# Kernel optimization log

Measured on AMD Instinct MI355X. Metric: run time of the kernel, lower is better.

The kernel has to match this reference:

```python
import jax, jax.numpy as jnp
import numpy as np

B, S, D, L = 16, 512, 256, 8192
DROP_P = 0.2


def setup_inputs() -> dict:
    key = jax.random.key(0)
    k1, k2, k3 = jax.random.split(key, 3)
    x = jax.random.normal(k1, (B, S, D), dtype=jnp.float32)
    label_emb = jax.random.normal(k2, (B, L, D), dtype=jnp.float32)
    mask = jax.random.uniform(k3, (B, S)) < 0.9
    return {"x": x, "mask": mask, "label_emb": label_emb}


def reference(x, mask, label_emb):
    # scores = x @ label_emb^T : [B, S, L]
    scores = jnp.einsum("bsd,bld->bsl", x, label_emb)
    # softmax over label dim (last)
    probs = jax.nn.softmax(scores, axis=-1)
    # post-softmax token masking (non-standard order, faithful to original)
    probs = jnp.where(mask[:, :, None], probs, jnp.zeros((), probs.dtype))
    # dropout (training=True in original), deterministic key for reproducibility
    keep = jax.random.bernoulli(jax.random.key(42), 1.0 - DROP_P, probs.shape)
    probs = jnp.where(keep, probs / (1.0 - DROP_P), jnp.zeros((), probs.dtype))
    # attention pooling: scores^T @ x : [B, L, D]
    return jnp.einsum("bsl,bsd->bld", probs, x)
```

## Files before the change

### kernel.cpp

```cpp
#include <hip/hip_runtime.h>
#include <stdint.h>
#include <stddef.h>

#define B_ 16
#define S_ 512
#define D_ 256
#define L_ 8192

typedef unsigned short u16;
typedef _Float16 f16;
typedef f16 f16x4 __attribute__((ext_vector_type(4)));
typedef f16 f16x8 __attribute__((ext_vector_type(8)));
typedef float f32x4 __attribute__((ext_vector_type(4)));

__device__ __forceinline__ void gl16(const void* g, void* l) {
  __builtin_amdgcn_global_load_lds(
      (const __attribute__((address_space(1))) unsigned int*)g,
      (__attribute__((address_space(3))) unsigned int*)l, 16, 0, 0);
}

__device__ __forceinline__ uint32_t rotl32(uint32_t x, int r) {
  return (x << r) | (x >> (32 - r));
}
__device__ __forceinline__ bool drop_keep(uint32_t j) {
  const uint32_t k0 = 0u, k1 = 42u, k2 = 0x1BD11BDAu ^ k0 ^ k1;
  uint32_t v0 = 0u + k0;
  uint32_t v1 = j + k1;
#define TF_R(r) { v0 += v1; v1 = rotl32(v1, (r)); v1 ^= v0; }
  TF_R(13) TF_R(15) TF_R(26) TF_R(6)
  v0 += k1; v1 += k2 + 1u;
  TF_R(17) TF_R(29) TF_R(16) TF_R(24)
  v0 += k2; v1 += k0 + 2u;
  TF_R(13) TF_R(15) TF_R(26) TF_R(6)
  v0 += k0; v1 += k1 + 3u;
  TF_R(17) TF_R(29) TF_R(16) TF_R(24)
  v0 += k1; v1 += k2 + 4u;
  TF_R(13) TF_R(15) TF_R(26) TF_R(6)
  v0 += k2; v1 += k0 + 5u;
#undef TF_R
  uint32_t bits = v0 ^ v1;
  float u = __uint_as_float((bits >> 9) | 0x3f800000u) - 1.0f;
  return u < 0.8f;
}

__global__ __launch_bounds__(256)
void conv16_kernel(const float* __restrict__ src, f16* __restrict__ dst, int n) {
  int i = (blockIdx.x * 256 + threadIdx.x) * 8;
  if (i >= n) return;
  float4 a = *(const float4*)&src[i];
  float4 b = *(const float4*)&src[i + 4];
  f16x8 o;
  o[0] = (f16)a.x; o[1] = (f16)a.y; o[2] = (f16)a.z; o[3] = (f16)a.w;
  o[4] = (f16)b.x; o[5] = (f16)b.y; o[6] = (f16)b.z; o[7] = (f16)b.w;
  *(f16x8*)&dst[i] = o;
}

__global__ __launch_bounds__(256)
void xt16_kernel(const float* __restrict__ x, f16* __restrict__ xT) {
  const int b = blockIdx.z, sb = blockIdx.x * 32, db = blockIdx.y * 32;
  __shared__ float t[32][33];
  const int tid = threadIdx.x;
  const int r = tid >> 3, c4 = (tid & 7) * 4;
  float4 v = *(const float4*)&x[((size_t)b * S_ + sb + r) * D_ + db + c4];
  t[r][c4] = v.x; t[r][c4 + 1] = v.y; t[r][c4 + 2] = v.z; t[r][c4 + 3] = v.w;
  __syncthreads();
  const int dr = tid >> 3, s4 = (tid & 7) * 4;
  f16x4 o;
#pragma unroll
  for (int j = 0; j < 4; ++j) o[j] = (f16)t[s4 + j][dr];
  *(f16x4*)&xT[((size_t)b * D_ + db + dr) * S_ + sb + s4] = o;
}

__global__ __launch_bounds__(256)
void gemm1t_f16(const f16* __restrict__ eh, const f16* __restrict__ xh,
                float* __restrict__ scoresT, float2* __restrict__ partials,
                uint32_t* __restrict__ kb) {
  __shared__ __align__(16) f16 As[2][4096];
  __shared__ __align__(16) f16 Bs[2][4096];
  __shared__ float pmaxA[128][2];
  __shared__ float psumA[128][2];

  const int tid = threadIdx.x;
  const int lane = tid & 63, wave = tid >> 6;
  const int b = blockIdx.z, lt = blockIdx.x * 128, st = blockIdx.y * 128;

  const int lm = lane & 15, kq = lane >> 4;
  const int wm = (wave & 1) * 64, wn = (wave >> 1) * 64;
  const int ca = (wave & 1) * 4, cb = (wave >> 1) * 4;

  const int srow = lane & 15, sko = (lane >> 4) * 8;
  auto stage = [&](int bi, int k0) {
#pragma unroll
    for (int i = 0; i < 2; ++i) {
      const int c = wave * 2 + i;
      gl16(eh + ((size_t)b * L_ + lt + c * 16 + srow) * D_ + k0 + sko,
           (char*)As[bi] + c * 1024 + lane * 16);
      gl16(xh + ((size_t)b * S_ + st + c * 16 + srow) * D_ + k0 + sko,
           (char*)Bs[bi] + c * 1024 + lane * 16);
    }
  };

  const int q0 = (tid & 1) * 2;
  const int ml = lt + (tid >> 1);
  uint32_t wlo = 0, whi = 0;

  f32x4 acc[4][4] = {};

  stage(0, 0);
  __syncthreads();
  int bi = 0;
  for (int t = 0; t < 8; ++t) {
    if (t < 7) stage(bi ^ 1, (t + 1) * 32);

    {
      const int c = t & 3, q = q0 + (t >> 2);
      const uint32_t base =
          (uint32_t)(b * S_ + st + 32 * c + 8 * q) * (uint32_t)L_ +
          (uint32_t)ml;
      uint32_t byte = 0;
#pragma unroll
      for (int j = 0; j < 8; ++j)
        byte |= (uint32_t)drop_keep(base + (uint32_t)j * L_) << j;
      if (t < 4) wlo |= byte << (8 * c);
      else       whi |= byte << (8 * c);
    }

    f16x8 fa[4], fb[4];
#pragma unroll
    for (int mi = 0; mi < 4; ++mi)
      fa[mi] = *(const f16x8*)&As[bi][((ca + mi) * 64 + kq * 16 + lm) * 8];
#pragma unroll
    for (int ni = 0; ni < 4; ++ni)
      fb[ni] = *(const f16x8*)&Bs[bi][((cb + ni) * 64 + kq * 16 + lm) * 8];
#pragma unroll
    for (int mi = 0; mi < 4; ++mi)
#pragma unroll
      for (int ni = 0; ni < 4; ++ni)
        acc[mi][ni] = __builtin_amdgcn_mfma_f32_16x16x32_f16(
            fa[mi], fb[ni], acc[mi][ni], 0, 0, 0);
    __syncthreads();
    bi ^= 1;
  }

  {
    uint32_t* kp = kb + ((size_t)b * L_ + ml) * 16 + blockIdx.y;
    kp[q0 * 4] = wlo;
    kp[(q0 + 1) * 4] = whi;
  }

#pragma unroll
  for (int mi = 0; mi < 4; ++mi)
#pragma unroll
    for (int ni = 0; ni < 4; ++ni) {
      const int l0 = wm + mi * 16 + kq * 4;
      const int s = wn + ni * 16 + lm;
      float* sp = scoresT + ((size_t)b * L_ + lt + l0) * S_ + st + s;
#pragma unroll
      for (int r = 0; r < 4; ++r) sp[(size_t)r * S_] = acc[mi][ni][r];
    }

  float cmax[4];
#pragma unroll
  for (int ni = 0; ni < 4; ++ni) {
    float v = acc[0][ni][0];
#pragma unroll
    for (int mi = 0; mi < 4; ++mi)
#pragma unroll
      for (int r = 0; r < 4; ++r) v = fmaxf(v, acc[mi][ni][r]);
    cmax[ni] = v;
  }
#pragma unroll
  for (int ni = 0; ni < 4; ++ni) {
    cmax[ni] = fmaxf(cmax[ni], __shfl_xor(cmax[ni], 16, 64));
    cmax[ni] = fmaxf(cmax[ni], __shfl_xor(cmax[ni], 32, 64));
  }
  if (kq == 0) {
#pragma unroll
    for (int ni = 0; ni < 4; ++ni) pmaxA[wn + ni * 16 + lm][wave & 1] = cmax[ni];
  }
  __syncthreads();
  float colm[4];
#pragma unroll
  for (int ni = 0; ni < 4; ++ni) {
    const int s = wn + ni * 16 + lm;
    colm[ni] = fmaxf(pmaxA[s][0], pmaxA[s][1]);
  }
  float psum[4] = {};
#pragma unroll
  for (int ni = 0; ni < 4; ++ni)
#pragma unroll
    for (int mi = 0; mi < 4; ++mi)
#pragma unroll
      for (int r = 0; r < 4; ++r)
        psum[ni] += __expf(acc[mi][ni][r] - colm[ni]);
#pragma unroll
  for (int ni = 0; ni < 4; ++ni) {
    psum[ni] += __shfl_xor(psum[ni], 16, 64);
    psum[ni] += __shfl_xor(psum[ni], 32, 64);
  }
  if (kq == 0) {
#pragma unroll
    for (int ni = 0; ni < 4; ++ni) psumA[wn + ni * 16 + lm][wave & 1] = psum[ni];
  }
  __syncthreads();
  if (tid < 128) {
    float m = fmaxf(pmaxA[tid][0], pmaxA[tid][1]);
    float Z = psumA[tid][0] + psumA[tid][1];
    partials[((size_t)b * 64 + blockIdx.x) * S_ + st + tid] = make_float2(m, Z);
  }
}

__global__ __launch_bounds__(256)
void combine_kernel(const float2* __restrict__ partials,
                    const int* __restrict__ mask, float2* __restrict__ stats) {
  const int idx = blockIdx.x * 256 + threadIdx.x;
  const int b = idx / S_, si = idx - b * S_;
  float m = -3.402823466e38f, Z = 0.f;
  for (int t = 0; t < 64; ++t) {
    float2 p = partials[((size_t)b * 64 + t) * S_ + si];
    if (p.x > m) {
      Z = Z * __expf(m - p.x) + p.y;
      m = p.x;
    } else {
      Z += p.y * __expf(p.x - m);
    }
  }
  float f = (mask[idx] != 0) ? (1.25f / Z) : 0.0f;
  stats[idx] = make_float2(m, f);
}

__global__ __launch_bounds__(512)
void gemm2_fused(const float* __restrict__ scoresT, const f16* __restrict__ xT,
                 const float2* __restrict__ stats,
                 const uint32_t* __restrict__ kb, float* __restrict__ out) {
  __shared__ __align__(16) f16 Bs[2][8192];
  __shared__ float2 stat_s[S_];

  const int tid = threadIdx.x;
  const int lane = tid & 63, wave = tid >> 6;
  const int b = blockIdx.z, lt = blockIdx.x * 128;

  stat_s[tid] = stats[b * S_ + tid];

  const int lm = lane & 15, kq = lane >> 4;
  const int l_loc = wave * 16 + lm;

  const int srow = lane & 15, sko = (lane >> 4) * 8;
  const size_t xb_base = (size_t)b * D_ * S_;
  auto stage = [&](int bi, int k0) {
#pragma unroll
    for (int i = 0; i < 2; ++i) {
      const int c = wave * 2 + i;
      gl16(xT + xb_base + (size_t)(c * 16 + srow) * S_ + k0 + sko,
           (char*)Bs[bi] + c * 1024 + lane * 16);
    }
  };

  const float* srowp =
      scoresT + ((size_t)b * L_ + lt + l_loc) * S_ + kq * 8;

  const uint4 kwv = *(const uint4*)(kb + ((size_t)b * L_ + lt + l_loc) * 16 +
                                    kq * 4);
  const uint32_t kwa[4] = {kwv.x, kwv.y, kwv.z, kwv.w};

  f32x4 acc[16] = {};

  f32x4 sv0 = *(const f32x4*)&srowp[0];
  f32x4 sv1 = *(const f32x4*)&srowp[4];
  stage(0, 0);
  __syncthreads();
#pragma unroll
  for (int kg = 0; kg < 4; ++kg) {
#pragma unroll
    for (int c = 0; c < 4; ++c) {
      const int kk = kg * 4 + c;
      const int k0 = kk * 32;
      const int bi = kk & 1;
      f32x4 nv0, nv1;
      if (kk < 15) {
        stage(bi ^ 1, k0 + 32);
        nv0 = *(const f32x4*)&srowp[k0 + 32];
        nv1 = *(const f32x4*)&srowp[k0 + 36];
      }

      float pv[8];
#pragma unroll
      for (int j = 0; j < 4; ++j) {
        const float2 mf = stat_s[k0 + kq * 8 + j];
        pv[j] = __expf(sv0[j] - mf.x) * mf.y;
      }
#pragma unroll
      for (int j = 0; j < 4; ++j) {
        const float2 mf = stat_s[k0 + kq * 8 + 4 + j];
        pv[4 + j] = __expf(sv1[j] - mf.x) * mf.y;
      }
      const uint32_t mbyte = (kwa[kg] >> (c * 8)) & 0xffu;
      f16x8 fa;
#pragma unroll
      for (int j = 0; j < 8; ++j)
        fa[j] = ((mbyte >> j) & 1u) ? (f16)pv[j] : (f16)0.f;

#pragma unroll
      for (int ni = 0; ni < 16; ++ni) {
        const f16x8 fb = *(const f16x8*)&Bs[bi][(ni * 64 + kq * 16 + lm) * 8];
        acc[ni] = __builtin_amdgcn_mfma_f32_16x16x32_f16(fa, fb, acc[ni], 0, 0, 0);
      }
      __syncthreads();
      if (kk < 15) { sv0 = nv0; sv1 = nv1; }
    }
  }

#pragma unroll
  for (int ni = 0; ni < 16; ++ni) {
    const int n = ni * 16 + lm;
    float* op = out + ((size_t)b * L_ + lt + wave * 16 + kq * 4) * D_ + n;
#pragma unroll
    for (int r = 0; r < 4; ++r) op[(size_t)r * D_] = acc[ni][r];
  }
}

extern "C" void kernel_launch(void* const* d_in, const int* in_sizes, int n_in,
                              void* d_out, int out_size, void* d_ws, size_t ws_size,
                              hipStream_t stream) {
  const float* x = (const float*)d_in[0];
  const int* mask = (const int*)d_in[1];
  const float* E = (const float*)d_in[2];
  float* out = (float*)d_out;

  char* ws = (char*)d_ws;
  const size_t nE = (size_t)B_ * L_ * D_;
  const size_t nX = (size_t)B_ * S_ * D_;
  size_t o = 0;
  f16* Eh = (f16*)(ws + o); o += nE * 2;
  f16* Xh = (f16*)(ws + o); o += nX * 2;
  f16* XT = (f16*)(ws + o); o += nX * 2;
  float2* stats = (float2*)(ws + o); o += (size_t)B_ * S_ * 8;
  float2* partials = (float2*)(ws + o); o += (size_t)B_ * 64 * S_ * 8;
  uint32_t* kb = (uint32_t*)(ws + o); o += (size_t)B_ * L_ * 16 * 4;
  float* scoresT = (float*)(ws + o);

  conv16_kernel<<<dim3((unsigned)(nE / 8 / 256)), 256, 0, stream>>>(E, Eh, (int)nE);
  conv16_kernel<<<dim3((unsigned)(nX / 8 / 256)), 256, 0, stream>>>(x, Xh, (int)nX);
  xt16_kernel<<<dim3(S_ / 32, D_ / 32, B_), 256, 0, stream>>>(x, XT);

  gemm1t_f16<<<dim3(L_ / 128, S_ / 128, B_), 256, 0, stream>>>(
      Eh, Xh, scoresT, partials, kb);
  combine_kernel<<<dim3(B_ * S_ / 256), 256, 0, stream>>>(partials, mask, stats);
  gemm2_fused<<<dim3(L_ / 128, 1, B_), 512, 0, stream>>>(scoresT, XT, stats, kb, out);
}
```

Before: 523.7 us.

## Redistribute dropout hash work across conv, gemm1 and gemm2 kernels

Dropout mask generation is now split three ways. The fp16 conversion kernel for the label embeddings hashes the first S-block, only the blockIdx.y==1 gemm1 blocks hash the second, and gemm2 computes the last two S-blocks inline instead of reading them from the kb buffer. The rotate uses an alignbit builtin, and the float-based keep compare becomes an integer threshold compare. The aim is to balance ALU-heavy Threefry hashing against memory-bound and MFMA-bound phases, which leaves gemm1 blocks unevenly loaded and adds hash ALU work inside the gemm2 inner loop.

After: 529.9 us. Within noise of the previous version (+1.2%).

```diff
diff --git a/kernel.cpp b/kernel.cpp
--- a/kernel.cpp
+++ b/kernel.cpp
@@ -20,7 +20,11 @@
 }
 
 __device__ __forceinline__ uint32_t rotl32(uint32_t x, int r) {
+#if __has_builtin(__builtin_amdgcn_alignbit)
+  return __builtin_amdgcn_alignbit(x, x, (32 - r) & 31);
+#else
   return (x << r) | (x >> (32 - r));
+#endif
 }
 __device__ __forceinline__ bool drop_keep(uint32_t j) {
   const uint32_t k0 = 0u, k1 = 42u, k2 = 0x1BD11BDAu ^ k0 ^ k1;
@@ -38,9 +42,8 @@
   TF_R(13) TF_R(15) TF_R(26) TF_R(6)
   v0 += k2; v1 += k0 + 5u;
 #undef TF_R
-  uint32_t bits = v0 ^ v1;
-  float u = __uint_as_float((bits >> 9) | 0x3f800000u) - 1.0f;
-  return u < 0.8f;
+  const uint32_t bits = v0 ^ v1;
+  return (bits >> 9) < 0x666667u;
 }
 
 __global__ __launch_bounds__(256)
@@ -56,6 +59,35 @@
 }
 
 __global__ __launch_bounds__(256)
+void conv16e_kernel(const float* __restrict__ src, f16* __restrict__ dst,
+                    uint32_t* __restrict__ kb) {
+  const int tg = blockIdx.x * 256 + threadIdx.x;
+  const int i = tg * 8;
+  float4 a = *(const float4*)&src[i];
+  float4 b = *(const float4*)&src[i + 4];
+  f16x8 o;
+  o[0] = (f16)a.x; o[1] = (f16)a.y; o[2] = (f16)a.z; o[3] = (f16)a.w;
+  o[4] = (f16)b.x; o[5] = (f16)b.y; o[6] = (f16)b.z; o[7] = (f16)b.w;
+  *(f16x8*)&dst[i] = o;
+
+  if (tg < B_ * L_ * 4) {
+    const int bb = tg >> 15;
+    const int rem = tg & 32767;
+    const int l = rem >> 2, q = rem & 3;
+    uint32_t w = 0;
+#pragma unroll
+    for (int c = 0; c < 4; ++c) {
+      const uint32_t base =
+          (uint32_t)(bb * S_ + 32 * c + 8 * q) * (uint32_t)L_ + (uint32_t)l;
+#pragma unroll
+      for (int j = 0; j < 8; ++j)
+        w |= (uint32_t)drop_keep(base + (uint32_t)j * L_) << (c * 8 + j);
+    }
+    kb[((size_t)bb * L_ + l) * 16 + q * 4] = w;
+  }
+}
+
+__global__ __launch_bounds__(256)
 void xt16_kernel(const float* __restrict__ x, f16* __restrict__ xT) {
   const int b = blockIdx.z, sb = blockIdx.x * 32, db = blockIdx.y * 32;
   __shared__ float t[32][33];
@@ -100,6 +132,7 @@
     }
   };
 
+  const bool do_hash = (blockIdx.y == 1);
   const int q0 = (tid & 1) * 2;
   const int ml = lt + (tid >> 1);
   uint32_t wlo = 0, whi = 0;
@@ -112,7 +145,7 @@
   for (int t = 0; t < 8; ++t) {
     if (t < 7) stage(bi ^ 1, (t + 1) * 32);
 
-    {
+    if (do_hash) {
       const int c = t & 3, q = q0 + (t >> 2);
       const uint32_t base =
           (uint32_t)(b * S_ + st + 32 * c + 8 * q) * (uint32_t)L_ +
@@ -142,7 +175,7 @@
     bi ^= 1;
   }
 
-  {
+  if (do_hash) {
     uint32_t* kp = kb + ((size_t)b * L_ + ml) * 16 + blockIdx.y;
     kp[q0 * 4] = wlo;
     kp[(q0 + 1) * 4] = whi;
@@ -244,6 +277,8 @@
 
   const int lm = lane & 15, kq = lane >> 4;
   const int l_loc = wave * 16 + lm;
+  const uint32_t gbase =
+      (uint32_t)(b * S_) * (uint32_t)L_ + (uint32_t)(lt + l_loc);
 
   const int srow = lane & 15, sko = (lane >> 4) * 8;
   const size_t xb_base = (size_t)b * D_ * S_;
@@ -259,9 +294,9 @@
   const float* srowp =
       scoresT + ((size_t)b * L_ + lt + l_loc) * S_ + kq * 8;
 
-  const uint4 kwv = *(const uint4*)(kb + ((size_t)b * L_ + lt + l_loc) * 16 +
+  const uint2 kwv = *(const uint2*)(kb + ((size_t)b * L_ + lt + l_loc) * 16 +
                                     kq * 4);
-  const uint32_t kwa[4] = {kwv.x, kwv.y, kwv.z, kwv.w};
+  const uint32_t kwa[2] = {kwv.x, kwv.y};
 
   f32x4 acc[16] = {};
 
@@ -283,6 +318,18 @@
         nv1 = *(const f32x4*)&srowp[k0 + 36];
       }
 
+      uint32_t mbyte;
+      if (kg < 2) {
+        mbyte = (kwa[kg] >> (c * 8)) & 0xffu;
+      } else {
+        const uint32_t hbase = gbase + (uint32_t)(k0 + kq * 8) * (uint32_t)L_;
+        uint32_t mb = 0;
+#pragma unroll
+        for (int j = 0; j < 8; ++j)
+          mb |= (uint32_t)drop_keep(hbase + (uint32_t)j * L_) << j;
+        mbyte = mb;
+      }
+
       float pv[8];
 #pragma unroll
       for (int j = 0; j < 4; ++j) {
@@ -294,7 +341,6 @@
         const float2 mf = stat_s[k0 + kq * 8 + 4 + j];
         pv[4 + j] = __expf(sv1[j] - mf.x) * mf.y;
       }
-      const uint32_t mbyte = (kwa[kg] >> (c * 8)) & 0xffu;
       f16x8 fa;
 #pragma unroll
       for (int j = 0; j < 8; ++j)
@@ -339,7 +385,7 @@
   uint32_t* kb = (uint32_t*)(ws + o); o += (size_t)B_ * L_ * 16 * 4;
   float* scoresT = (float*)(ws + o);
 
-  conv16_kernel<<<dim3((unsigned)(nE / 8 / 256)), 256, 0, stream>>>(E, Eh, (int)nE);
+  conv16e_kernel<<<dim3((unsigned)(nE / 8 / 256)), 256, 0, stream>>>(E, Eh, kb);
   conv16_kernel<<<dim3((unsigned)(nX / 8 / 256)), 256, 0, stream>>>(x, Xh, (int)nX);
   xt16_kernel<<<dim3(S_ / 32, D_ / 32, B_), 256, 0, stream>>>(x, XT);
 
```
